# Kernel tuning notes

Hardware: AMD Instinct MI355X
Metric: run time of the kernel (lower is better)

## Reference

```python
import jax, jax.numpy as jnp
import numpy as np
import math

H = 8  # num_heads

def setup_inputs() -> dict:
    key = jax.random.key(0)
    ks = jax.random.split(key, 12)
    B, N, M, k = 2, 8192, 8192, 32
    dq, dk, dv = 256, 256, 256
    s = 1.0 / math.sqrt(dq)
    inp = {
        'Q': jax.random.normal(ks[0], (B, N, dq), dtype=jnp.float32),
        'K': jax.random.normal(ks[1], (B, M, dk), dtype=jnp.float32),
        'neighbours': jax.random.randint(ks[2], (B, N, k), 0, M),
        'Wq': jax.random.normal(ks[3], (dq, dv), dtype=jnp.float32) * s,
        'bq': jnp.zeros((dv,), dtype=jnp.float32),
        'Wk': jax.random.normal(ks[4], (dk, dv), dtype=jnp.float32) * s,
        'bk': jnp.zeros((dv,), dtype=jnp.float32),
        'Wv': jax.random.normal(ks[5], (dk, dv), dtype=jnp.float32) * s,
        'bv': jnp.zeros((dv,), dtype=jnp.float32),
        'Wo': jax.random.normal(ks[6], (dv, dv), dtype=jnp.float32) * (1.0 / math.sqrt(dv)),
        'bo': jnp.zeros((dv,), dtype=jnp.float32),
    }
    return inp

def reference(Q, K, neighbours, Wq, bq, Wk, bk, Wv, bv, Wo, bo):
    B, N, _ = Q.shape
    dv = Wq.shape[1]
    ds = dv // H
    # project and split heads (contiguous channel chunks == reshape)
    Qh = (Q @ Wq + bq).reshape(B, N, H, ds)            # [B,N,H,ds]
    Kh = (K @ Wk + bk).reshape(B, -1, H, ds)           # [B,M,H,ds]
    Vh = (K @ Wv + bv).reshape(B, -1, H, ds)           # [B,M,H,ds]
    # gather per-node kNN neighbour keys/values: [B,N,k,H,ds]
    gather = jax.vmap(lambda x, idx: x[idx])
    Kn = gather(Kh, neighbours)
    Vn = gather(Vh, neighbours)
    # scale uses full latent size (faithful to original), not head dim
    scale = 1.0 / math.sqrt(dv)
    E = jnp.einsum('bnhd,bnkhd->bnhk', Qh, Kn) * scale  # [B,N,H,k]
    A = jax.nn.softmax(E, axis=-1)
    AV = jnp.einsum('bnhk,bnkhd->bnhd', A, Vn).reshape(B, N, dv)
    return AV @ Wo + bo
```

## Files before the change

### kernel.cpp

```cpp
#include <hip/hip_runtime.h>
#include <hip/hip_bf16.h>
#include <stdint.h>

typedef unsigned short u16;
typedef __attribute__((ext_vector_type(8))) short short8;
typedef __attribute__((ext_vector_type(4))) float f32x4;

__device__ __forceinline__ u16 f2bf(float f) {
    union { float f; unsigned int i; } v; v.f = f;
    unsigned int b = v.i;
    return (u16)((b + 0x7FFFu + ((b >> 16) & 1u)) >> 16);
}

__device__ __forceinline__ short8 cvt8(float4 a, float4 b) {
    union { __hip_bfloat162 h[4]; short8 s; } u;
    u.h[0] = __float22bfloat162_rn(make_float2(a.x, a.y));
    u.h[1] = __float22bfloat162_rn(make_float2(a.z, a.w));
    u.h[2] = __float22bfloat162_rn(make_float2(b.x, b.y));
    u.h[3] = __float22bfloat162_rn(make_float2(b.z, b.w));
    return u.s;
}

typedef const __attribute__((address_space(1))) void* as1cv;
typedef __attribute__((address_space(3))) void* as3v;
__device__ __forceinline__ void gload16(const void* g, void* l) {
    __builtin_amdgcn_global_load_lds((as1cv)g, (as3v)l, 16, 0, 0);
}

__device__ __forceinline__ void up2(unsigned int v, float& lo, float& hi) {
    union { unsigned int i; float f; } a, b;
    a.i = v << 16; b.i = v & 0xffff0000u;
    lo = a.f; hi = b.f;
}

__global__ __launch_bounds__(256) void wprep(
    const float* __restrict__ W0, const float* __restrict__ W1,
    const float* __restrict__ W2, const float* __restrict__ W3,
    u16* __restrict__ T0, u16* __restrict__ T1,
    u16* __restrict__ T2, u16* __restrict__ T3)
{
    const float* W = blockIdx.z == 0 ? W0 : blockIdx.z == 1 ? W1 : blockIdx.z == 2 ? W2 : W3;
    u16*        T  = blockIdx.z == 0 ? T0 : blockIdx.z == 1 ? T1 : blockIdx.z == 2 ? T2 : T3;
    __shared__ u16 ts[64][65];
    int k0 = blockIdx.x * 64, n0 = blockIdx.y * 64;
    int t = threadIdx.x;
    int r = t >> 2, cq = (t & 3) * 16;
    const float4* src = reinterpret_cast<const float4*>(W + (k0 + r) * 256 + n0 + cq);
    for (int u = 0; u < 4; ++u) {
        float4 v = src[u];
        int c = cq + u * 4;
        ts[r][c + 0] = f2bf(v.x); ts[r][c + 1] = f2bf(v.y);
        ts[r][c + 2] = f2bf(v.z); ts[r][c + 3] = f2bf(v.w);
    }
    __syncthreads();
    u16* dst = T + (n0 + r) * 256 + k0 + cq;
    for (int u = 0; u < 16; ++u) dst[u] = ts[cq + u][r];
}

__global__ __launch_bounds__(256) void gemm_proj(
    const float* __restrict__ Q, const float* __restrict__ K,
    const u16* __restrict__ Wtq, const u16* __restrict__ Wtk, const u16* __restrict__ Wtv,
    const float* __restrict__ bq, const float* __restrict__ bk, const float* __restrict__ bv,
    u16* __restrict__ Qh, u16* __restrict__ Kh, u16* __restrict__ Vh)
{
    int z = blockIdx.z;
    const float* Af   = (z == 0) ? Q   : K;
    const u16*   Wt   = (z == 0) ? Wtq : (z == 1) ? Wtk : Wtv;
    const float* bias = (z == 0) ? bq  : (z == 1) ? bk  : bv;
    u16*         C    = (z == 0) ? Qh  : (z == 1) ? Kh  : Vh;

    __shared__ float Asf[64 * 64];
    __shared__ u16   Bs[256 * 64];

    int t = threadIdx.x;
    int lane = t & 63, w = t >> 6;
    int row0 = blockIdx.x * 64;
    int wr = (w >> 1) * 32, wc = (w & 1) * 128;
    int qd = lane >> 4, md = lane & 15;

    f32x4 acc[2][8] = {};

    for (int kt = 0; kt < 256; kt += 64) {
#pragma unroll
        for (int u = 0; u < 4; ++u) {
            int chunk = w * 4 + u;
            int s = chunk * 64 + lane;
            int r = s >> 4, c = s & 15;
            gload16(Af + (size_t)(row0 + r) * 256 + kt + ((c ^ (r & 15)) * 4),
                    (char*)Asf + chunk * 1024);
        }
#pragma unroll
        for (int u = 0; u < 8; ++u) {
            int chunk = w * 8 + u;
            int s = chunk * 64 + lane;
            int r = s >> 3, c = s & 7;
            gload16(Wt + (size_t)r * 256 + kt + ((c ^ (r & 7)) * 8),
                    (char*)Bs + chunk * 1024);
        }
        __syncthreads();
#pragma unroll
        for (int ks = 0; ks < 64; ks += 32) {
            short8 af[2], bf[8];
#pragma unroll
            for (int i = 0; i < 2; ++i) {
                int ar = wr + i * 16 + md;
                int c0 = (ks >> 2) + qd * 2;
                int x = ar & 15;
                float4 fa0 = reinterpret_cast<const float4*>(Asf)[ar * 16 + (c0 ^ x)];
                float4 fa1 = reinterpret_cast<const float4*>(Asf)[ar * 16 + ((c0 + 1) ^ x)];
                af[i] = cvt8(fa0, fa1);
            }
#pragma unroll
            for (int j = 0; j < 8; ++j) {
                int br = wc + j * 16 + md;
                int slot = ((ks >> 3) + qd) ^ (br & 7);
                bf[j] = reinterpret_cast<const short8*>(Bs)[br * 8 + slot];
            }
#pragma unroll
            for (int i = 0; i < 2; ++i)
#pragma unroll
                for (int j = 0; j < 8; ++j)
                    acc[i][j] = __builtin_amdgcn_mfma_f32_16x16x32_bf16(
                        af[i], bf[j], acc[i][j], 0, 0, 0);
        }
        __syncthreads();
    }

#pragma unroll
    for (int i = 0; i < 2; ++i)
#pragma unroll
        for (int j = 0; j < 8; ++j) {
            int col = wc + j * 16 + md;
            float b = bias[col];
#pragma unroll
            for (int r = 0; r < 4; ++r) {
                int row = row0 + wr + i * 16 + qd * 4 + r;
                C[(size_t)row * 256 + col] = f2bf(acc[i][j][r] + b);
            }
        }
}

__global__ __launch_bounds__(256) void gemm_out(
    const u16* __restrict__ Ab, const u16* __restrict__ Wt,
    const float* __restrict__ bias, float* __restrict__ Cout)
{
    __shared__ u16 As[64 * 64];
    __shared__ u16 Bs[128 * 64];

    int t = threadIdx.x;
    int lane = t & 63, w = t >> 6;
    int row0 = blockIdx.x * 64, col0 = blockIdx.y * 128;
    int wr = (w >> 1) * 32, wc = (w & 1) * 64;
    int qd = lane >> 4, md = lane & 15;

    f32x4 acc[2][4] = {};

    for (int kt = 0; kt < 256; kt += 64) {
#pragma unroll
        for (int u = 0; u < 2; ++u) {
            int chunk = w * 2 + u;
            int s = chunk * 64 + lane;
            int r = s >> 3, c = s & 7;
            gload16(Ab + (size_t)(row0 + r) * 256 + kt + ((c ^ (r & 7)) * 8),
                    (char*)As + chunk * 1024);
        }
#pragma unroll
        for (int u = 0; u < 4; ++u) {
            int chunk = w * 4 + u;
            int s = chunk * 64 + lane;
            int r = s >> 3, c = s & 7;
            gload16(Wt + (size_t)(col0 + r) * 256 + kt + ((c ^ (r & 7)) * 8),
                    (char*)Bs + chunk * 1024);
        }
        __syncthreads();
#pragma unroll
        for (int ks = 0; ks < 64; ks += 32) {
            short8 af[2], bf[4];
#pragma unroll
            for (int i = 0; i < 2; ++i) {
                int ar = wr + i * 16 + md;
                int slot = ((ks >> 3) + qd) ^ (ar & 7);
                af[i] = reinterpret_cast<const short8*>(As)[ar * 8 + slot];
            }
#pragma unroll
            for (int j = 0; j < 4; ++j) {
                int br = wc + j * 16 + md;
                int slot = ((ks >> 3) + qd) ^ (br & 7);
                bf[j] = reinterpret_cast<const short8*>(Bs)[br * 8 + slot];
            }
#pragma unroll
            for (int i = 0; i < 2; ++i)
#pragma unroll
                for (int j = 0; j < 4; ++j)
                    acc[i][j] = __builtin_amdgcn_mfma_f32_16x16x32_bf16(
                        af[i], bf[j], acc[i][j], 0, 0, 0);
        }
        __syncthreads();
    }

#pragma unroll
    for (int i = 0; i < 2; ++i)
#pragma unroll
        for (int j = 0; j < 4; ++j) {
            int col = col0 + wc + j * 16 + md;
            float b = bias[col];
#pragma unroll
            for (int r = 0; r < 4; ++r) {
                int row = row0 + wr + i * 16 + qd * 4 + r;
                Cout[(size_t)row * 256 + col] = acc[i][j][r] + b;
            }
        }
}

__device__ __forceinline__ void attn_map2(int blk, int w, int& row, int& hf) {
    int g = blk & 7;
    int batch = g >> 2;
    hf = (g >> 1) & 1;
    int cb = (blk >> 3) * 2 + (g & 1);
    row = batch * 8192 + cb * 4 + w;
}

__global__ __launch_bounds__(256) void attn_fused(
    const u16* __restrict__ Qh, const u16* __restrict__ Kh,
    const u16* __restrict__ Vh, const int* __restrict__ nbr,
    u16* __restrict__ AVb)
{
    __shared__ int jbs[4][32];

    int t = threadIdx.x;
    int w = t >> 6, lane = t & 63;
    int row, hf;
    attn_map2(blockIdx.x, w, row, hf);
    int bbase = (row >> 13) << 13;

    int c4 = lane & 15;
    int jg = lane >> 4;

    if (lane < 32) {
        int ji = nbr[(size_t)row * 32 + lane];
        jbs[w][lane] = (bbase + ji) * 256 + hf * 128;
    }

    float qf[8];
    {
        uint4 qw = *reinterpret_cast<const uint4*>(Qh + (size_t)row * 256 + hf * 128 + c4 * 8);
        up2(qw.x, qf[0], qf[1]); up2(qw.y, qf[2], qf[3]);
        up2(qw.z, qf[4], qf[5]); up2(qw.w, qf[6], qf[7]);
    }

    int off[8];
#pragma unroll
    for (int u = 0; u < 8; ++u) off[u] = jbs[w][jg * 8 + u];

    uint4 kw[8];
#pragma unroll
    for (int u = 0; u < 8; ++u)
        kw[u] = *reinterpret_cast<const uint4*>(Kh + (size_t)off[u] + c4 * 8);

    uint4 vv[8];
#pragma unroll
    for (int u = 0; u < 8; ++u)
        vv[u] = *reinterpret_cast<const uint4*>(Vh + (size_t)off[u] + c4 * 8);

    float e8[8];
#pragma unroll
    for (int u = 0; u < 8; ++u) {
        float k0, k1;
        float p = 0.f;
        up2(kw[u].x, k0, k1); p = fmaf(qf[0], k0, p); p = fmaf(qf[1], k1, p);
        up2(kw[u].y, k0, k1); p = fmaf(qf[2], k0, p); p = fmaf(qf[3], k1, p);
        up2(kw[u].z, k0, k1); p = fmaf(qf[4], k0, p); p = fmaf(qf[5], k1, p);
        up2(kw[u].w, k0, k1); p = fmaf(qf[6], k0, p); p = fmaf(qf[7], k1, p);
        p += __shfl_xor(p, 1);
        p += __shfl_xor(p, 2);
        e8[u] = p * 0.0625f;
    }

    float m = e8[0];
#pragma unroll
    for (int jj = 1; jj < 8; ++jj) m = fmaxf(m, e8[jj]);
    m = fmaxf(m, __shfl_xor(m, 16));
    m = fmaxf(m, __shfl_xor(m, 32));
    float s = 0.f;
#pragma unroll
    for (int jj = 0; jj < 8; ++jj) { e8[jj] = __expf(e8[jj] - m); s += e8[jj]; }
    s += __shfl_xor(s, 16);
    s += __shfl_xor(s, 32);
    float rs = 1.0f / s;

    float acc[8] = {};
#pragma unroll
    for (int u = 0; u < 8; ++u) {
        float v0, v1;
        float wgt = e8[u] * rs;
        up2(vv[u].x, v0, v1); acc[0] = fmaf(wgt, v0, acc[0]); acc[1] = fmaf(wgt, v1, acc[1]);
        up2(vv[u].y, v0, v1); acc[2] = fmaf(wgt, v0, acc[2]); acc[3] = fmaf(wgt, v1, acc[3]);
        up2(vv[u].z, v0, v1); acc[4] = fmaf(wgt, v0, acc[4]); acc[5] = fmaf(wgt, v1, acc[5]);
        up2(vv[u].w, v0, v1); acc[6] = fmaf(wgt, v0, acc[6]); acc[7] = fmaf(wgt, v1, acc[7]);
    }
#pragma unroll
    for (int u = 0; u < 8; ++u) {
        acc[u] += __shfl_xor(acc[u], 16);
        acc[u] += __shfl_xor(acc[u], 32);
    }

    if (lane < 16) {
        union { __hip_bfloat162 h2[4]; uint4 u4; } o;
        o.h2[0] = __float22bfloat162_rn(make_float2(acc[0], acc[1]));
        o.h2[1] = __float22bfloat162_rn(make_float2(acc[2], acc[3]));
        o.h2[2] = __float22bfloat162_rn(make_float2(acc[4], acc[5]));
        o.h2[3] = __float22bfloat162_rn(make_float2(acc[6], acc[7]));
        *reinterpret_cast<uint4*>(AVb + (size_t)row * 256 + hf * 128 + c4 * 8) = o.u4;
    }
}

extern "C" void kernel_launch(void* const* d_in, const int* in_sizes, int n_in,
                              void* d_out, int out_size, void* d_ws, size_t ws_size,
                              hipStream_t stream) {
    const float* Q   = (const float*)d_in[0];
    const float* K   = (const float*)d_in[1];
    const int*   nbr = (const int*)d_in[2];
    const float* Wq  = (const float*)d_in[3];
    const float* bq  = (const float*)d_in[4];
    const float* Wk  = (const float*)d_in[5];
    const float* bk  = (const float*)d_in[6];
    const float* Wv  = (const float*)d_in[7];
    const float* bv  = (const float*)d_in[8];
    const float* Wo  = (const float*)d_in[9];
    const float* bo  = (const float*)d_in[10];
    float* out = (float*)d_out;

    char* ws = (char*)d_ws;
    size_t off = 0;
    auto alloc = [&](size_t bytes) -> void* {
        void* p = ws + off;
        off += (bytes + 255) & ~(size_t)255;
        return p;
    };
    const size_t MN = 16384;
    u16* Wtq = (u16*)alloc(256 * 256 * 2);
    u16* Wtk = (u16*)alloc(256 * 256 * 2);
    u16* Wtv = (u16*)alloc(256 * 256 * 2);
    u16* Wto = (u16*)alloc(256 * 256 * 2);
    u16* Qh  = (u16*)alloc(MN * 256 * 2);
    u16* Kh  = (u16*)alloc(MN * 256 * 2);
    u16* Vh  = (u16*)alloc(MN * 256 * 2);
    u16* AVb = (u16*)alloc(MN * 256 * 2);

    wprep<<<dim3(4, 4, 4), 256, 0, stream>>>(Wq, Wk, Wv, Wo, Wtq, Wtk, Wtv, Wto);
    gemm_proj<<<dim3(256, 1, 3), 256, 0, stream>>>(Q, K, Wtq, Wtk, Wtv,
                                                   bq, bk, bv, Qh, Kh, Vh);
    attn_fused<<<dim3(8192), 256, 0, stream>>>(Qh, Kh, Vh, nbr, AVb);
    gemm_out<<<dim3(256, 2), 256, 0, stream>>>(AVb, Wto, bo, out);
}
```

Before: 146.1 us.

## Fuse kNN attention with output projection, keeping AV tile in LDS

```diff
diff --git a/kernel.cpp b/kernel.cpp
--- a/kernel.cpp
+++ b/kernel.cpp
@@ -105,9 +105,9 @@
             for (int i = 0; i < 2; ++i) {
                 int ar = wr + i * 16 + md;
                 int c0 = (ks >> 2) + qd * 2;
-                int x = ar & 15;
-                float4 fa0 = reinterpret_cast<const float4*>(Asf)[ar * 16 + (c0 ^ x)];
-                float4 fa1 = reinterpret_cast<const float4*>(Asf)[ar * 16 + ((c0 + 1) ^ x)];
+                int xx = ar & 15;
+                float4 fa0 = reinterpret_cast<const float4*>(Asf)[ar * 16 + (c0 ^ xx)];
+                float4 fa1 = reinterpret_cast<const float4*>(Asf)[ar * 16 + ((c0 + 1) ^ xx)];
                 af[i] = cvt8(fa0, fa1);
             }
 #pragma unroll
@@ -140,177 +140,165 @@
         }
 }
 
-__global__ __launch_bounds__(256) void gemm_out(
-    const u16* __restrict__ Ab, const u16* __restrict__ Wt,
-    const float* __restrict__ bias, float* __restrict__ Cout)
+__global__ __launch_bounds__(256) void attn_out(
+    const u16* __restrict__ Qh, const u16* __restrict__ Kh,
+    const u16* __restrict__ Vh, const int* __restrict__ nbr,
+    const u16* __restrict__ Wto, const float* __restrict__ bo,
+    float* __restrict__ out)
 {
-    __shared__ u16 As[64 * 64];
-    __shared__ u16 Bs[128 * 64];
+    __shared__ int jbs[16][32];
+    __shared__ alignas(16) char avbB[8192];
+    __shared__ alignas(16) u16 Bs[256 * 64];
 
     int t = threadIdx.x;
-    int lane = t & 63, w = t >> 6;
-    int row0 = blockIdx.x * 64, col0 = blockIdx.y * 128;
-    int wr = (w >> 1) * 32, wc = (w & 1) * 64;
+    int w = t >> 6, lane = t & 63;
+    int c4 = lane & 15;
+    int jg = lane >> 4;
     int qd = lane >> 4, md = lane & 15;
 
-    f32x4 acc[2][4] = {};
-
-    for (int kt = 0; kt < 256; kt += 64) {
-#pragma unroll
-        for (int u = 0; u < 2; ++u) {
-            int chunk = w * 2 + u;
+    int bid = blockIdx.x;
+    int batch = bid >> 9;
+    int R0 = batch * 8192 + (bid & 511) * 16;
+    int bbase = batch * 8192;
+
+#pragma unroll
+    for (int q = 0; q < 2; ++q) {
+        int s = t + q * 256;
+        int rl = s >> 5, li = s & 31;
+        int ji = nbr[(size_t)(R0 + rl) * 32 + li];
+        jbs[rl][li] = (bbase + ji) * 256;
+    }
+    __syncthreads();
+
+    int hf = w >> 1;
+    int rl0 = (w & 1) * 8;
+
+#pragma unroll 1
+    for (int j = 0; j < 8; ++j) {
+        int rl = rl0 + j;
+        int row = R0 + rl;
+
+        float qf[8];
+        {
+            uint4 qw = *reinterpret_cast<const uint4*>(
+                Qh + (size_t)row * 256 + hf * 128 + c4 * 8);
+            up2(qw.x, qf[0], qf[1]); up2(qw.y, qf[2], qf[3]);
+            up2(qw.z, qf[4], qf[5]); up2(qw.w, qf[6], qf[7]);
+        }
+
+        int off[8];
+#pragma unroll
+        for (int u = 0; u < 8; ++u) off[u] = jbs[rl][jg * 8 + u] + hf * 128;
+
+        uint4 kw[8];
+#pragma unroll
+        for (int u = 0; u < 8; ++u)
+            kw[u] = *reinterpret_cast<const uint4*>(Kh + (size_t)off[u] + c4 * 8);
+
+        uint4 vv[8];
+#pragma unroll
+        for (int u = 0; u < 8; ++u)
+            vv[u] = *reinterpret_cast<const uint4*>(Vh + (size_t)off[u] + c4 * 8);
+
+        float e8[8];
+#pragma unroll
+        for (int u = 0; u < 8; ++u) {
+            float k0, k1;
+            float p = 0.f;
+            up2(kw[u].x, k0, k1); p = fmaf(qf[0], k0, p); p = fmaf(qf[1], k1, p);
+            up2(kw[u].y, k0, k1); p = fmaf(qf[2], k0, p); p = fmaf(qf[3], k1, p);
+            up2(kw[u].z, k0, k1); p = fmaf(qf[4], k0, p); p = fmaf(qf[5], k1, p);
+            up2(kw[u].w, k0, k1); p = fmaf(qf[6], k0, p); p = fmaf(qf[7], k1, p);
+            p += __shfl_xor(p, 1);
+            p += __shfl_xor(p, 2);
+            e8[u] = p * 0.0625f;
+        }
+
+        float m = e8[0];
+#pragma unroll
+        for (int jj = 1; jj < 8; ++jj) m = fmaxf(m, e8[jj]);
+        m = fmaxf(m, __shfl_xor(m, 16));
+        m = fmaxf(m, __shfl_xor(m, 32));
+        float s = 0.f;
+#pragma unroll
+        for (int jj = 0; jj < 8; ++jj) { e8[jj] = __expf(e8[jj] - m); s += e8[jj]; }
+        s += __shfl_xor(s, 16);
+        s += __shfl_xor(s, 32);
+        float rs = 1.0f / s;
+
+        float acc[8] = {};
+#pragma unroll
+        for (int u = 0; u < 8; ++u) {
+            float v0, v1;
+            float wgt = e8[u] * rs;
+            up2(vv[u].x, v0, v1); acc[0] = fmaf(wgt, v0, acc[0]); acc[1] = fmaf(wgt, v1, acc[1]);
+            up2(vv[u].y, v0, v1); acc[2] = fmaf(wgt, v0, acc[2]); acc[3] = fmaf(wgt, v1, acc[3]);
+            up2(vv[u].z, v0, v1); acc[4] = fmaf(wgt, v0, acc[4]); acc[5] = fmaf(wgt, v1, acc[5]);
+            up2(vv[u].w, v0, v1); acc[6] = fmaf(wgt, v0, acc[6]); acc[7] = fmaf(wgt, v1, acc[7]);
+        }
+#pragma unroll
+        for (int u = 0; u < 8; ++u) {
+            acc[u] += __shfl_xor(acc[u], 16);
+            acc[u] += __shfl_xor(acc[u], 32);
+        }
+
+        if (lane < 16) {
+            union { __hip_bfloat162 h2[4]; uint4 u4; } o;
+            o.h2[0] = __float22bfloat162_rn(make_float2(acc[0], acc[1]));
+            o.h2[1] = __float22bfloat162_rn(make_float2(acc[2], acc[3]));
+            o.h2[2] = __float22bfloat162_rn(make_float2(acc[4], acc[5]));
+            o.h2[3] = __float22bfloat162_rn(make_float2(acc[6], acc[7]));
+            int C = hf * 16 + lane;
+            int ktg = C >> 3, c = C & 7;
+            *reinterpret_cast<uint4*>(
+                avbB + ktg * 2048 + rl * 128 + ((c ^ (rl & 7)) * 16)) = o.u4;
+        }
+    }
+    __syncthreads();
+
+    f32x4 oacc[4] = {};
+
+#pragma unroll 1
+    for (int kt_i = 0; kt_i < 4; ++kt_i) {
+        int kt = kt_i * 64;
+#pragma unroll
+        for (int u = 0; u < 8; ++u) {
+            int chunk = w * 8 + u;
             int s = chunk * 64 + lane;
             int r = s >> 3, c = s & 7;
-            gload16(Ab + (size_t)(row0 + r) * 256 + kt + ((c ^ (r & 7)) * 8),
-                    (char*)As + chunk * 1024);
-        }
-#pragma unroll
-        for (int u = 0; u < 4; ++u) {
-            int chunk = w * 4 + u;
-            int s = chunk * 64 + lane;
-            int r = s >> 3, c = s & 7;
-            gload16(Wt + (size_t)(col0 + r) * 256 + kt + ((c ^ (r & 7)) * 8),
+            gload16(Wto + (size_t)r * 256 + kt + ((c ^ (r & 7)) * 8),
                     (char*)Bs + chunk * 1024);
         }
         __syncthreads();
+        const char* As_t = avbB + kt_i * 2048;
 #pragma unroll
         for (int ks = 0; ks < 64; ks += 32) {
-            short8 af[2], bf[4];
-#pragma unroll
-            for (int i = 0; i < 2; ++i) {
-                int ar = wr + i * 16 + md;
-                int slot = ((ks >> 3) + qd) ^ (ar & 7);
-                af[i] = reinterpret_cast<const short8*>(As)[ar * 8 + slot];
+            int slot = ((ks >> 3) + qd) ^ (md & 7);
+            short8 af = *reinterpret_cast<const short8*>(As_t + (md * 8 + slot) * 16);
+            short8 bf[4];
+#pragma unroll
+            for (int j2 = 0; j2 < 4; ++j2) {
+                int br = w * 64 + j2 * 16 + md;
+                int slotb = ((ks >> 3) + qd) ^ (br & 7);
+                bf[j2] = reinterpret_cast<const short8*>(Bs)[br * 8 + slotb];
             }
 #pragma unroll
-            for (int j = 0; j < 4; ++j) {
-                int br = wc + j * 16 + md;
-                int slot = ((ks >> 3) + qd) ^ (br & 7);
-                bf[j] = reinterpret_cast<const short8*>(Bs)[br * 8 + slot];
-            }
-#pragma unroll
-            for (int i = 0; i < 2; ++i)
-#pragma unroll
-                for (int j = 0; j < 4; ++j)
-                    acc[i][j] = __builtin_amdgcn_mfma_f32_16x16x32_bf16(
-                        af[i], bf[j], acc[i][j], 0, 0, 0);
+            for (int j2 = 0; j2 < 4; ++j2)
+                oacc[j2] = __builtin_amdgcn_mfma_f32_16x16x32_bf16(
+                    af, bf[j2], oacc[j2], 0, 0, 0);
         }
         __syncthreads();
     }
 
 #pragma unroll
-    for (int i = 0; i < 2; ++i)
-#pragma unroll
-        for (int j = 0; j < 4; ++j) {
-            int col = col0 + wc + j * 16 + md;
-            float b = bias[col];
-#pragma unroll
-            for (int r = 0; r < 4; ++r) {
-                int row = row0 + wr + i * 16 + qd * 4 + r;
-                Cout[(size_t)row * 256 + col] = acc[i][j][r] + b;
-            }
-        }
-}
-
-__device__ __forceinline__ void attn_map2(int blk, int w, int& row, int& hf) {
-    int g = blk & 7;
-    int batch = g >> 2;
-    hf = (g >> 1) & 1;
-    int cb = (blk >> 3) * 2 + (g & 1);
-    row = batch * 8192 + cb * 4 + w;
-}
-
-__global__ __launch_bounds__(256) void attn_fused(
-    const u16* __restrict__ Qh, const u16* __restrict__ Kh,
-    const u16* __restrict__ Vh, const int* __restrict__ nbr,
-    u16* __restrict__ AVb)
-{
-    __shared__ int jbs[4][32];
-
-    int t = threadIdx.x;
-    int w = t >> 6, lane = t & 63;
-    int row, hf;
-    attn_map2(blockIdx.x, w, row, hf);
-    int bbase = (row >> 13) << 13;
-
-    int c4 = lane & 15;
-    int jg = lane >> 4;
-
-    if (lane < 32) {
-        int ji = nbr[(size_t)row * 32 + lane];
-        jbs[w][lane] = (bbase + ji) * 256 + hf * 128;
-    }
-
-    float qf[8];
-    {
-        uint4 qw = *reinterpret_cast<const uint4*>(Qh + (size_t)row * 256 + hf * 128 + c4 * 8);
-        up2(qw.x, qf[0], qf[1]); up2(qw.y, qf[2], qf[3]);
-        up2(qw.z, qf[4], qf[5]); up2(qw.w, qf[6], qf[7]);
-    }
-
-    int off[8];
-#pragma unroll
-    for (int u = 0; u < 8; ++u) off[u] = jbs[w][jg * 8 + u];
-
-    uint4 kw[8];
-#pragma unroll
-    for (int u = 0; u < 8; ++u)
-        kw[u] = *reinterpret_cast<const uint4*>(Kh + (size_t)off[u] + c4 * 8);
-
-    uint4 vv[8];
-#pragma unroll
-    for (int u = 0; u < 8; ++u)
-        vv[u] = *reinterpret_cast<const uint4*>(Vh + (size_t)off[u] + c4 * 8);
-
-    float e8[8];
-#pragma unroll
-    for (int u = 0; u < 8; ++u) {
-        float k0, k1;
-        float p = 0.f;
-        up2(kw[u].x, k0, k1); p = fmaf(qf[0], k0, p); p = fmaf(qf[1], k1, p);
-        up2(kw[u].y, k0, k1); p = fmaf(qf[2], k0, p); p = fmaf(qf[3], k1, p);
-        up2(kw[u].z, k0, k1); p = fmaf(qf[4], k0, p); p = fmaf(qf[5], k1, p);
-        up2(kw[u].w, k0, k1); p = fmaf(qf[6], k0, p); p = fmaf(qf[7], k1, p);
-        p += __shfl_xor(p, 1);
-        p += __shfl_xor(p, 2);
-        e8[u] = p * 0.0625f;
-    }
-
-    float m = e8[0];
-#pragma unroll
-    for (int jj = 1; jj < 8; ++jj) m = fmaxf(m, e8[jj]);
-    m = fmaxf(m, __shfl_xor(m, 16));
-    m = fmaxf(m, __shfl_xor(m, 32));
-    float s = 0.f;
-#pragma unroll
-    for (int jj = 0; jj < 8; ++jj) { e8[jj] = __expf(e8[jj] - m); s += e8[jj]; }
-    s += __shfl_xor(s, 16);
-    s += __shfl_xor(s, 32);
-    float rs = 1.0f / s;
-
-    float acc[8] = {};
-#pragma unroll
-    for (int u = 0; u < 8; ++u) {
-        float v0, v1;
-        float wgt = e8[u] * rs;
-        up2(vv[u].x, v0, v1); acc[0] = fmaf(wgt, v0, acc[0]); acc[1] = fmaf(wgt, v1, acc[1]);
-        up2(vv[u].y, v0, v1); acc[2] = fmaf(wgt, v0, acc[2]); acc[3] = fmaf(wgt, v1, acc[3]);
-        up2(vv[u].z, v0, v1); acc[4] = fmaf(wgt, v0, acc[4]); acc[5] = fmaf(wgt, v1, acc[5]);
-        up2(vv[u].w, v0, v1); acc[6] = fmaf(wgt, v0, acc[6]); acc[7] = fmaf(wgt, v1, acc[7]);
-    }
-#pragma unroll
-    for (int u = 0; u < 8; ++u) {
-        acc[u] += __shfl_xor(acc[u], 16);
-        acc[u] += __shfl_xor(acc[u], 32);
-    }
-
-    if (lane < 16) {
-        union { __hip_bfloat162 h2[4]; uint4 u4; } o;
-        o.h2[0] = __float22bfloat162_rn(make_float2(acc[0], acc[1]));
-        o.h2[1] = __float22bfloat162_rn(make_float2(acc[2], acc[3]));
-        o.h2[2] = __float22bfloat162_rn(make_float2(acc[4], acc[5]));
-        o.h2[3] = __float22bfloat162_rn(make_float2(acc[6], acc[7]));
-        *reinterpret_cast<uint4*>(AVb + (size_t)row * 256 + hf * 128 + c4 * 8) = o.u4;
+    for (int j2 = 0; j2 < 4; ++j2) {
+        int col = w * 64 + j2 * 16 + md;
+        float b = bo[col];
+#pragma unroll
+        for (int rr = 0; rr < 4; ++rr) {
+            int row = R0 + qd * 4 + rr;
+            out[(size_t)row * 256 + col] = oacc[j2][rr] + b;
+        }
     }
 }
 
@@ -345,11 +333,9 @@
     u16* Qh  = (u16*)alloc(MN * 256 * 2);
     u16* Kh  = (u16*)alloc(MN * 256 * 2);
     u16* Vh  = (u16*)alloc(MN * 256 * 2);
-    u16* AVb = (u16*)alloc(MN * 256 * 2);
 
     wprep<<<dim3(4, 4, 4), 256, 0, stream>>>(Wq, Wk, Wv, Wo, Wtq, Wtk, Wtv, Wto);
     gemm_proj<<<dim3(256, 1, 3), 256, 0, stream>>>(Q, K, Wtq, Wtk, Wtv,
                                                    bq, bk, bv, Qh, Kh, Vh);
-    attn_fused<<<dim3(8192), 256, 0, stream>>>(Qh, Kh, Vh, nbr, AVb);
-    gemm_out<<<dim3(256, 2), 256, 0, stream>>>(AVb, Wto, bo, out);
-}
+    attn_out<<<dim3(1024), 256, 0, stream>>>(Qh, Kh, Vh, nbr, Wto, bo, out);
+}
```

Measured after the change: 176.1 us. 1.21x slower.
